# Performance work log

Measured on AMD Instinct MI355X. Metric: run time of the kernel, lower is better.

## Reference

```python
import jax, jax.numpy as jnp
import numpy as np
import math

B, T, D, H = 4, 1024, 1024, 16
DK = D // H
TAU_THRESH = 0.3


def setup_inputs() -> dict:
    key = jax.random.key(0)
    ks = jax.random.split(key, 13)
    s = 1.0 / math.sqrt(D)
    return {
        "x": jax.random.normal(ks[0], (B, T, D), dtype=jnp.float32),
        "Wq": jax.random.normal(ks[1], (D, D), dtype=jnp.float32) * s,
        "bq": jax.random.normal(ks[2], (D,), dtype=jnp.float32) * s,
        "Wk": jax.random.normal(ks[3], (D, D), dtype=jnp.float32) * s,
        "bk": jax.random.normal(ks[4], (D,), dtype=jnp.float32) * s,
        "Wv": jax.random.normal(ks[5], (D, D), dtype=jnp.float32) * s,
        "bv": jax.random.normal(ks[6], (D,), dtype=jnp.float32) * s,
        "Wo": jax.random.normal(ks[7], (D, D), dtype=jnp.float32) * s,
        "bo": jax.random.normal(ks[8], (D,), dtype=jnp.float32) * s,
        "Wg1": jax.random.normal(ks[9], (1, D), dtype=jnp.float32) * s,
        "bg1": jax.random.normal(ks[10], (1,), dtype=jnp.float32) * s,
        "Wg2": jax.random.normal(ks[11], (1, D), dtype=jnp.float32) * s,
        "bg2": jax.random.normal(ks[12], (1,), dtype=jnp.float32) * s,
    }


def reference(x, Wq, bq, Wk, bk, Wv, bv, Wo, bo, Wg1, bg1, Wg2, bg2):
    b, t, d = x.shape
    # projections (torch Linear: y = x @ W.T + b)
    Q = (x @ Wq.T + bq).reshape(b, t, H, DK).transpose(0, 2, 1, 3)  # [B,H,T,dk]
    K = (x @ Wk.T + bk).reshape(b, t, H, DK).transpose(0, 2, 1, 3)
    V = (x @ Wv.T + bv).reshape(b, t, H, DK).transpose(0, 2, 1, 3)
    scores = jnp.einsum("bhqd,bhkd->bhqk", Q, K) / math.sqrt(DK)  # [B,H,T,T]
    # confidence gates from first-token query context [B, H*dk] = [B, D]
    context = Q[:, :, 0, :].reshape(b, d)
    q1 = jax.nn.sigmoid(context @ Wg1.T + bg1)  # [B,1]
    q2 = jax.nn.sigmoid(context @ Wg2.T + bg2)  # [B,1]
    c = jnp.clip(q1 * q2, 1e-8, 1.0)            # [B,1]
    tau = jnp.where(c < TAU_THRESH, 1.0 / c, jnp.ones_like(c)).reshape(b, 1, 1, 1)
    p = jax.nn.softmax(scores / tau, axis=-1)
    cb = c.reshape(b, 1, 1, 1)
    p_gated = cb * p + (1.0 - cb) * (1.0 / t)
    u = jnp.mean(1.0 - c, axis=-1, keepdims=True)  # [B,1]
    attn_out = jnp.einsum("bhqk,bhkd->bhqd", p_gated, V)
    attn_out = attn_out.transpose(0, 2, 1, 3).reshape(b, t, d)
    output = attn_out @ Wo.T + bo
    return output, u
```

## Files before the change

### kernel.cpp

```cpp
#include <hip/hip_runtime.h>
#include <stdint.h>

typedef short bf16x8 __attribute__((ext_vector_type(8)));
typedef float f32x4 __attribute__((ext_vector_type(4)));

#define MFMA_BF16(a, b, c) __builtin_amdgcn_mfma_f32_16x16x32_bf16((a), (b), (c), 0, 0, 0)

__device__ __forceinline__ short f2bf(float x) {
  union { float f; uint32_t u; } v; v.f = x;
  uint32_t r = (v.u + 0x7FFFu + ((v.u >> 16) & 1u)) >> 16;
  return (short)r;
}
__device__ __forceinline__ uint32_t rnd_bf_hi(float x) {
  union { float f; uint32_t u; } v; v.f = x;
  return v.u + 0x7FFFu + ((v.u >> 16) & 1u);
}
__device__ __forceinline__ uint32_t pack2bf(float a, float b) {
  return __builtin_amdgcn_perm(rnd_bf_hi(b), rnd_bf_hi(a), 0x07060302);
}
__device__ __forceinline__ float bfbits2f(uint32_t b16) {
  union { uint32_t u; float f; } v; v.u = b16 << 16; return v.f;
}
__device__ __forceinline__ float fexp2(float x) {
#if __has_builtin(__builtin_amdgcn_exp2f)
  return __builtin_amdgcn_exp2f(x);
#else
  return __expf(x * 0.6931471805599453f);
#endif
}
__device__ __forceinline__ void async16(const void* g, void* l) {
  __builtin_amdgcn_global_load_lds(
      (const __attribute__((address_space(1))) uint32_t*)g,
      (__attribute__((address_space(3))) uint32_t*)l, 16, 0, 0);
}

__global__ __launch_bounds__(256) void prep_k(
    const float* __restrict__ x, const float* __restrict__ Wq,
    const float* __restrict__ Wk, const float* __restrict__ Wv,
    const float* __restrict__ Wo, const float* __restrict__ bq,
    short* __restrict__ xb, short* __restrict__ Wqb, short* __restrict__ Wkb,
    short* __restrict__ Wvb, short* __restrict__ Wob, float* __restrict__ ctx) {
  __shared__ float xs[1024];
  const int bid = blockIdx.x;
  const int tid = threadIdx.x;
  if (bid < 8192) {
    const float* src; short* dst; int idx;
    if (bid < 4096) {
      src = x; dst = xb; idx = (bid << 8) + tid;
    } else {
      const int r = bid - 4096;
      const int z = r >> 10;
      src = (z == 0) ? Wq : (z == 1) ? Wk : (z == 2) ? Wv : Wo;
      dst = (z == 0) ? Wqb : (z == 1) ? Wkb : (z == 2) ? Wvb : Wob;
      idx = ((r & 1023) << 8) + tid;
    }
    float4 v = ((const float4*)src)[idx];
    short4 o;
    o.x = f2bf(v.x); o.y = f2bf(v.y); o.z = f2bf(v.z); o.w = f2bf(v.w);
    ((short4*)dst)[idx] = o;
  } else {
    const int r = bid - 8192;
    const int b = r >> 4;
    const int n0 = (r & 15) << 6;
    for (int i = tid; i < 1024; i += 256) xs[i] = x[b * 1048576 + i];
    __syncthreads();
    const int w = tid >> 6, lane = tid & 63;
    const float4* xv4 = (const float4*)xs;
    for (int rr = 0; rr < 16; ++rr) {
      const int n = n0 + (w << 4) + rr;
      const float4* wrow = (const float4*)(Wq + n * 1024);
      float p = 0.f;
#pragma unroll
      for (int c2 = 0; c2 < 4; ++c2) {
        float4 wv = wrow[lane + (c2 << 6)];
        float4 xv = xv4[lane + (c2 << 6)];
        p += xv.x * wv.x + xv.y * wv.y + xv.z * wv.z + xv.w * wv.w;
      }
#pragma unroll
      for (int off = 32; off; off >>= 1) p += __shfl_xor(p, off);
      if (lane == 0) ctx[b * 1024 + n] = p + bq[n];
    }
  }
}

__global__ __launch_bounds__(256) void gates_fin(const float* __restrict__ ctx,
                                                 const float* __restrict__ Wg1,
                                                 const float* __restrict__ bg1,
                                                 const float* __restrict__ Wg2,
                                                 const float* __restrict__ bg2,
                                                 float* __restrict__ gates,
                                                 float* __restrict__ u_out) {
  __shared__ float red[16];
  const int tid = threadIdx.x, w = tid >> 6, lane = tid & 63;
  for (int b = 0; b < 4; ++b) {
    float4 cv = ((const float4*)(ctx + b * 1024))[tid];
    float4 w1 = ((const float4*)Wg1)[tid];
    float4 w2 = ((const float4*)Wg2)[tid];
    float p1 = cv.x * w1.x + cv.y * w1.y + cv.z * w1.z + cv.w * w1.w;
    float p2 = cv.x * w2.x + cv.y * w2.y + cv.z * w2.z + cv.w * w2.w;
#pragma unroll
    for (int off = 32; off; off >>= 1) { p1 += __shfl_xor(p1, off); p2 += __shfl_xor(p2, off); }
    if (lane == 0) { red[w] = p1; red[8 + w] = p2; }
    __syncthreads();
    if (tid == 0) {
      float g1 = red[0] + red[1] + red[2] + red[3] + bg1[0];
      float g2 = red[8] + red[9] + red[10] + red[11] + bg2[0];
      float q1 = 1.f / (1.f + expf(-g1));
      float q2 = 1.f / (1.f + expf(-g2));
      float c = fminf(fmaxf(q1 * q2, 1e-8f), 1.0f);
      gates[b * 2 + 0] = c;
      gates[b * 2 + 1] = (c < 0.3f ? c : 1.0f) * 0.125f * 1.4426950408889634f;
      u_out[b] = 1.0f - c;
    }
    __syncthreads();
  }
}

template <bool SWP>
__device__ __forceinline__ void qkv_core128(
    const short* __restrict__ A, const short* __restrict__ W,
    const float* __restrict__ bias, short* __restrict__ out,
    short* As, short* Bs, int m0, int n0) {
  const int tid = threadIdx.x;
  const int w = tid >> 6, lane = tid & 63;
  const int m15 = lane & 15, quad = lane >> 4;
  const int wr = w >> 1, wc = w & 1;

  f32x4 acc[4][4];
#pragma unroll
  for (int i = 0; i < 4; ++i)
#pragma unroll
    for (int j = 0; j < 4; ++j) { f32x4 zz = {0.f, 0.f, 0.f, 0.f}; acc[i][j] = zz; }

  const int srow = (w << 5) + (lane >> 2);
  const int sxor = (srow >> 1) & 3;
  const int scol = (((lane & 3) ^ sxor) << 3);
  const short* ga0 = A + (m0 + srow) * 1024 + scol;
  const short* ga1 = ga0 + 16 * 1024;
  const short* gb0 = W + (n0 + srow) * 1024 + scol;
  const short* gb1 = gb0 + 16 * 1024;
  short* la0 = &As[srow * 32 + ((lane & 3) << 3)];
  short* la1 = la0 + 512;
  short* lb0 = &Bs[srow * 32 + ((lane & 3) << 3)];
  short* lb1 = lb0 + 512;

  async16(ga0, la0); async16(ga1, la1);
  async16(gb0, lb0); async16(gb1, lb1);
  __syncthreads();

  for (int kt = 0; kt < 32; ++kt) {
    const int buf = kt & 1;
    if (kt < 31) {
      const int nb = (buf ^ 1) << 12;
      const int off = (kt + 1) << 5;
      async16(ga0 + off, la0 + nb); async16(ga1 + off, la1 + nb);
      async16(gb0 + off, lb0 + nb); async16(gb1 + off, lb1 + nb);
    }
    const short* Ab = As + (buf << 12);
    const short* Bb = Bs + (buf << 12);
    bf16x8 a[4], b[4];
#pragma unroll
    for (int i = 0; i < 4; ++i) {
      const int ra = (wr << 6) + (i << 4) + m15;
      a[i] = *(const bf16x8*)(&Ab[ra * 32 + ((quad ^ ((ra >> 1) & 3)) << 3)]);
    }
#pragma unroll
    for (int j = 0; j < 4; ++j) {
      const int rb = (wc << 6) + (j << 4) + m15;
      b[j] = *(const bf16x8*)(&Bb[rb * 32 + ((quad ^ ((rb >> 1) & 3)) << 3)]);
    }
#pragma unroll
    for (int i = 0; i < 4; ++i)
#pragma unroll
      for (int j = 0; j < 4; ++j) {
        if (SWP) acc[i][j] = MFMA_BF16(b[j], a[i], acc[i][j]);
        else     acc[i][j] = MFMA_BF16(a[i], b[j], acc[i][j]);
      }
    if (kt < 31) __syncthreads();
  }

  if (SWP) {
#pragma unroll
    for (int j = 0; j < 4; ++j) {
      const int n = n0 + (wc << 6) + (j << 4) + (quad << 2);
      const float4 bv = *(const float4*)(bias + n);
      const int hh = n >> 6, dk0 = n & 63;
#pragma unroll
      for (int i = 0; i < 4; ++i) {
        const int m = m0 + (wr << 6) + (i << 4) + m15;
        const int bb = m >> 10, tt = m & 1023;
        uint2 st;
        st.x = pack2bf(acc[i][j][0] + bv.x, acc[i][j][1] + bv.y);
        st.y = pack2bf(acc[i][j][2] + bv.z, acc[i][j][3] + bv.w);
        *(uint2*)(out + (((bb << 4) + hh) << 16) + (tt << 6) + dk0) = st;
      }
    }
  } else {
#pragma unroll
    for (int j = 0; j < 4; ++j) {
      const int n = n0 + (wc << 6) + (j << 4) + m15;
      const float bv = bias[n];
      const int hh = n >> 6, dk = n & 63;
#pragma unroll
      for (int i = 0; i < 4; ++i) {
        const int m = m0 + (wr << 6) + (i << 4) + (quad << 2);
        const int bb = m >> 10, t0 = m & 1023;
        uint2 st;
        st.x = pack2bf(acc[i][j][0] + bv, acc[i][j][1] + bv);
        st.y = pack2bf(acc[i][j][2] + bv, acc[i][j][3] + bv);
        *(uint2*)(out + (((bb << 4) + hh) << 16) + (dk << 10) + t0) = st;
      }
    }
  }
}

__global__ __launch_bounds__(256) void gemm_qkv(
    const short* __restrict__ xb,
    const short* __restrict__ Wqb, const short* __restrict__ Wkb, const short* __restrict__ Wvb,
    const float* __restrict__ bq, const float* __restrict__ bk, const float* __restrict__ bv,
    short* __restrict__ Qh, short* __restrict__ Kh, short* __restrict__ Vt) {
  __shared__ short As[8192];
  __shared__ short Bs[8192];
  const int z = blockIdx.z;
  const int m0 = blockIdx.x << 7, n0 = blockIdx.y << 7;
  if (z == 0)      qkv_core128<true >(xb, Wqb, bq, Qh, As, Bs, m0, n0);
  else if (z == 1) qkv_core128<true >(xb, Wkb, bk, Kh, As, Bs, m0, n0);
  else             qkv_core128<false>(xb, Wvb, bv, Vt, As, Bs, m0, n0);
}

__global__ __launch_bounds__(256) void gemm_out(const short* __restrict__ Ab_,
                                                const short* __restrict__ Wo,
                                                const float* __restrict__ bo,
                                                float* __restrict__ Cout) {
  const int m0 = blockIdx.x << 7;
  const int n0 = blockIdx.y << 7;
  const int tid = threadIdx.x;
  const int w = tid >> 6, lane = tid & 63;
  const int m15 = lane & 15, quad = lane >> 4;
  const int wr = w >> 1, wc = w & 1;

  __shared__ short As[8192];
  __shared__ short Bs[8192];

  f32x4 acc[4][4];
#pragma unroll
  for (int i = 0; i < 4; ++i)
#pragma unroll
    for (int j = 0; j < 4; ++j) { f32x4 zz = {0.f, 0.f, 0.f, 0.f}; acc[i][j] = zz; }

  const int srow = (w << 5) + (lane >> 2);
  const int sxor = (srow >> 1) & 3;
  const int scol = (((lane & 3) ^ sxor) << 3);
  const short* ga0 = Ab_ + (m0 + srow) * 1024 + scol;
  const short* ga1 = ga0 + 16 * 1024;
  const short* gb0 = Wo + (n0 + srow) * 1024 + scol;
  const short* gb1 = gb0 + 16 * 1024;
  short* la0 = &As[srow * 32 + ((lane & 3) << 3)];
  short* la1 = la0 + 512;
  short* lb0 = &Bs[srow * 32 + ((lane & 3) << 3)];
  short* lb1 = lb0 + 512;

  async16(ga0, la0); async16(ga1, la1);
  async16(gb0, lb0); async16(gb1, lb1);
  __syncthreads();

  for (int kt = 0; kt < 32; ++kt) {
    const int buf = kt & 1;
    if (kt < 31) {
      const int nb = (buf ^ 1) << 12;
      const int off = (kt + 1) << 5;
      async16(ga0 + off, la0 + nb); async16(ga1 + off, la1 + nb);
      async16(gb0 + off, lb0 + nb); async16(gb1 + off, lb1 + nb);
    }
    const short* Ab = As + (buf << 12);
    const short* Bb = Bs + (buf << 12);
    bf16x8 a[4], b[4];
#pragma unroll
    for (int i = 0; i < 4; ++i) {
      const int ra = (wr << 6) + (i << 4) + m15;
      a[i] = *(const bf16x8*)(&Ab[ra * 32 + ((quad ^ ((ra >> 1) & 3)) << 3)]);
    }
#pragma unroll
    for (int j = 0; j < 4; ++j) {
      const int rb = (wc << 6) + (j << 4) + m15;
      b[j] = *(const bf16x8*)(&Bb[rb * 32 + ((quad ^ ((rb >> 1) & 3)) << 3)]);
    }
#pragma unroll
    for (int i = 0; i < 4; ++i)
#pragma unroll
      for (int j = 0; j < 4; ++j)
        acc[i][j] = MFMA_BF16(a[i], b[j], acc[i][j]);
    if (kt < 31) __syncthreads();
  }

#pragma unroll
  for (int j = 0; j < 4; ++j) {
    const int n = n0 + (wc << 6) + (j << 4) + m15;
    const float bb_ = bo[n];
#pragma unroll
    for (int i = 0; i < 4; ++i) {
      const int mb = m0 + (wr << 6) + (i << 4) + (quad << 2);
#pragma unroll
      for (int r = 0; r < 4; ++r)
        Cout[(mb + r) * 1024 + n] = acc[i][j][r] + bb_;
    }
  }
}

__global__ __launch_bounds__(256, 2) void attn_k(const short* __restrict__ Qh,
                                                 const short* __restrict__ Kh,
                                                 const short* __restrict__ Vt,
                                                 const float* __restrict__ gates,
                                                 short* __restrict__ attnb) {
  const int bh = blockIdx.x;
  const int b = bh >> 4, h = bh & 15;
  const int q0 = blockIdx.y << 7;
  const int tid = threadIdx.x;
  const int w = tid >> 6, lane = tid & 63;
  const int m15 = lane & 15, quad = lane >> 4;

  __shared__ short Ks[2][4096];
  __shared__ short Vs[3][4096];

  const short* ksrc = Kh + bh * 65536;
  const short* vsrc = Vt + bh * 65536;

  const float sl = gates[b * 2 + 1];

  const short* qsrcA = Qh + ((bh << 10) + q0 + (w << 4) + m15) * 64;
  const short* qsrcB = qsrcA + 64 * 64;
  const bf16x8 qA0 = *(const bf16x8*)(qsrcA + (quad << 3));
  const bf16x8 qA1 = *(const bf16x8*)(qsrcA + 32 + (quad << 3));
  const bf16x8 qB0 = *(const bf16x8*)(qsrcB + (quad << 3));
  const bf16x8 qB1 = *(const bf16x8*)(qsrcB + 32 + (quad << 3));

  const bf16x8 vone = {0x3F80, 0x3F80, 0x3F80, 0x3F80, 0x3F80, 0x3F80, 0x3F80, 0x3F80};

  const int off0 = tid, off1 = tid + 256;
  const int r0 = off0 >> 3, cb0 = (off0 & 7) ^ (r0 & 7);
  const int r1 = off1 >> 3, cb1 = (off1 & 7) ^ (r1 & 7);

#define STAGE(kv, kb, vb)                                                      \
  do {                                                                         \
    async16(ksrc + (((kv) << 6) + r0) * 64 + (cb0 << 3), &Ks[kb][off0 << 3]);  \
    async16(ksrc + (((kv) << 6) + r1) * 64 + (cb1 << 3), &Ks[kb][off1 << 3]);  \
    async16(vsrc + r0 * 1024 + ((kv) << 6) + (cb0 << 3), &Vs[vb][off0 << 3]);  \
    async16(vsrc + r1 * 1024 + ((kv) << 6) + (cb1 << 3), &Vs[vb][off1 << 3]);  \
  } while (0)

  STAGE(0, 0, 0);

  float lsumA = 0.f, lsumB = 0.f;
  f32x4 oA[4], oB[4], o_mv[4];
#pragma unroll
  for (int jd = 0; jd < 4; ++jd) {
    f32x4 zz = {0.f, 0.f, 0.f, 0.f};
    oA[jd] = zz; oB[jd] = zz; o_mv[jd] = zz;
  }

  const int srcA = ((quad & 1) << 5) + m15;
  const int srcB = srcA + 16;
  const bool selhi = (quad & 2) != 0;

#define BUILD_PF(pf, pk)                                                       \
  do {                                                                         \
    _Pragma("unroll")                                                          \
    for (int Hh = 0; Hh < 2; ++Hh) {                                           \
      uint32_t f[4];                                                           \
      _Pragma("unroll")                                                        \
      for (int rp = 0; rp < 2; ++rp) {                                         \
        uint32_t alo = (uint32_t)__shfl((int)pk[2 * Hh][rp], srcA);            \
        uint32_t ahi = (uint32_t)__shfl((int)pk[2 * Hh + 1][rp], srcA);        \
        uint32_t blo = (uint32_t)__shfl((int)pk[2 * Hh][rp], srcB);            \
        uint32_t bhi = (uint32_t)__shfl((int)pk[2 * Hh + 1][rp], srcB);        \
        f[rp]     = selhi ? ahi : alo;                                         \
        f[2 + rp] = selhi ? bhi : blo;                                         \
      }                                                                        \
      pf[Hh] = *(bf16x8*)f;                                                    \
    }                                                                          \
  } while (0)

#define PV_STEP(Vb, pfa, pfb)                                                  \
  do {                                                                         \
    _Pragma("unroll")                                                          \
    for (int jd = 0; jd < 4; ++jd) {                                           \
      const int row = (jd << 4) + m15;                                         \
      const int sw = row & 7;                                                  \
      bf16x8 v0 = *(const bf16x8*)((Vb) + (row << 6) + ((quad ^ sw) << 3));    \
      bf16x8 v1 = *(const bf16x8*)((Vb) + (row << 6) + (((quad + 4) ^ sw) << 3)); \
      oA[jd] = MFMA_BF16(v0, pfa[0], oA[jd]);                                  \
      oA[jd] = MFMA_BF16(v1, pfa[1], oA[jd]);                                  \
      oB[jd] = MFMA_BF16(v0, pfb[0], oB[jd]);                                  \
      oB[jd] = MFMA_BF16(v1, pfb[1], oB[jd]);                                  \
      o_mv[jd] = MFMA_BF16(v0, vone, o_mv[jd]);                                \
      o_mv[jd] = MFMA_BF16(v1, vone, o_mv[jd]);                                \
    }                                                                          \
  } while (0)

  bf16x8 pfpA[2], pfpB[2];
  pfpA[0] = (bf16x8){0,0,0,0,0,0,0,0}; pfpA[1] = pfpA[0];
  pfpB[0] = pfpA[0]; pfpB[1] = pfpA[0];

  for (int kv = 0; kv < 16; ++kv) {
    __syncthreads();
    if (kv < 15) STAGE(kv + 1, (kv + 1) & 1, (kv + 1) % 3);
    const short* Kb = &Ks[kv & 1][0];

    f32x4 sA[4], sB[4];
#pragma unroll
    for (int s = 0; s < 4; ++s) {
      const int row = (s << 4) + m15;
      const int sw = row & 7;
      bf16x8 a0 = *(const bf16x8*)(Kb + (row << 6) + ((quad ^ sw) << 3));
      bf16x8 a1 = *(const bf16x8*)(Kb + (row << 6) + (((quad + 4) ^ sw) << 3));
      f32x4 zA = {0.f, 0.f, 0.f, 0.f};
      zA = MFMA_BF16(a0, qA0, zA);
      zA = MFMA_BF16(a1, qA1, zA);
      sA[s] = zA;
      f32x4 zB = {0.f, 0.f, 0.f, 0.f};
      zB = MFMA_BF16(a0, qB0, zB);
      zB = MFMA_BF16(a1, qB1, zB);
      sB[s] = zB;
    }

    if (kv > 0) {
      const short* Vb = &Vs[(kv - 1) % 3][0];
      PV_STEP(Vb, pfpA, pfpB);
    }

    uint32_t pkA[4][2], pkB[4][2];
#pragma unroll
    for (int s = 0; s < 4; ++s) {
      float a0 = fexp2(sA[s][0] * sl);
      float a1 = fexp2(sA[s][1] * sl);
      float a2 = fexp2(sA[s][2] * sl);
      float a3 = fexp2(sA[s][3] * sl);
      lsumA += (a0 + a1) + (a2 + a3);
      pkA[s][0] = pack2bf(a0, a1);
      pkA[s][1] = pack2bf(a2, a3);
      float b0 = fexp2(sB[s][0] * sl);
      float b1 = fexp2(sB[s][1] * sl);
      float b2 = fexp2(sB[s][2] * sl);
      float b3 = fexp2(sB[s][3] * sl);
      lsumB += (b0 + b1) + (b2 + b3);
      pkB[s][0] = pack2bf(b0, b1);
      pkB[s][1] = pack2bf(b2, b3);
    }

    bf16x8 pfA[2], pfB[2];
    BUILD_PF(pfA, pkA);
    BUILD_PF(pfB, pkB);
    pfpA[0] = pfA[0]; pfpA[1] = pfA[1];
    pfpB[0] = pfB[0]; pfpB[1] = pfB[1];
  }

  {
    const short* Vb = &Vs[15 % 3][0];
    PV_STEP(Vb, pfpA, pfpB);
  }
#undef STAGE
#undef BUILD_PF
#undef PV_STEP

  float lA = lsumA;
  lA += __shfl_xor(lA, 16);
  lA += __shfl_xor(lA, 32);
  float lB = lsumB;
  lB += __shfl_xor(lB, 16);
  lB += __shfl_xor(lB, 32);

  const float cg = gates[b * 2 + 0];
  const float sc0A = cg / lA;
  const float sc0B = cg / lB;
  const float coef = (1.0f - cg) * (1.0f / 1024.0f);
  const int qrowA = q0 + (w << 4) + m15;
  short* orowA = attnb + ((b << 10) + qrowA) * 1024 + (h << 6);
  short* orowB = orowA + 64 * 1024;
#pragma unroll
  for (int jd = 0; jd < 4; ++jd) {
    uint2 stA;
    stA.x = pack2bf(sc0A * oA[jd][0] + coef * o_mv[jd][0],
                    sc0A * oA[jd][1] + coef * o_mv[jd][1]);
    stA.y = pack2bf(sc0A * oA[jd][2] + coef * o_mv[jd][2],
                    sc0A * oA[jd][3] + coef * o_mv[jd][3]);
    *(uint2*)(orowA + (jd << 4) + (quad << 2)) = stA;
    uint2 stB;
    stB.x = pack2bf(sc0B * oB[jd][0] + coef * o_mv[jd][0],
                    sc0B * oB[jd][1] + coef * o_mv[jd][1]);
    stB.y = pack2bf(sc0B * oB[jd][2] + coef * o_mv[jd][2],
                    sc0B * oB[jd][3] + coef * o_mv[jd][3]);
    *(uint2*)(orowB + (jd << 4) + (quad << 2)) = stB;
  }
}

extern "C" void kernel_launch(void* const* d_in, const int* in_sizes, int n_in,
                              void* d_out, int out_size, void* d_ws, size_t ws_size,
                              hipStream_t stream) {
  const float* x   = (const float*)d_in[0];
  const float* Wq  = (const float*)d_in[1];
  const float* bq  = (const float*)d_in[2];
  const float* Wk  = (const float*)d_in[3];
  const float* bk  = (const float*)d_in[4];
  const float* Wv  = (const float*)d_in[5];
  const float* bv  = (const float*)d_in[6];
  const float* Wo  = (const float*)d_in[7];
  const float* bo  = (const float*)d_in[8];
  const float* Wg1 = (const float*)d_in[9];
  const float* bg1 = (const float*)d_in[10];
  const float* Wg2 = (const float*)d_in[11];
  const float* bg2 = (const float*)d_in[12];
  float* out = (float*)d_out;

  char* ws = (char*)d_ws;
  short* xb   = (short*)(ws + 0);
  short* Wqb  = (short*)(ws + 8388608);
  short* Wkb  = (short*)(ws + 10485760);
  short* Wvb  = (short*)(ws + 12582912);
  short* Wob  = (short*)(ws + 14680064);
  short* Qh   = (short*)(ws + 16777216);
  short* Kh   = (short*)(ws + 25165824);
  short* Vt   = (short*)(ws + 33554432);
  short* attb = (short*)(ws + 41943040);
  float* ctx  = (float*)(ws + 50331648);
  float* gat  = (float*)(ws + 50348032);

  prep_k<<<8256, 256, 0, stream>>>(x, Wq, Wk, Wv, Wo, bq,
                                   xb, Wqb, Wkb, Wvb, Wob, ctx);
  gates_fin<<<1, 256, 0, stream>>>(ctx, Wg1, bg1, Wg2, bg2, gat, out + 4194304);

  gemm_qkv<<<dim3(32, 8, 3), 256, 0, stream>>>(xb, Wqb, Wkb, Wvb, bq, bk, bv,
                                               Qh, Kh, Vt);
  attn_k<<<dim3(64, 8), 256, 0, stream>>>(Qh, Kh, Vt, gat, attb);
  gemm_out<<<dim3(32, 8), 256, 0, stream>>>(attb, Wob, bo, out);
}
```

Before: 215.9 us.

## Fuse fp32-to-bf16 conversion into GEMM tile loads and merge gate kernels

Drops the separate conversion pass that wrote bf16 copies of x and all four weight matrices. The QKV and output GEMMs now load fp32 tiles into registers, round them to bf16 and store them into the swizzled LDS double buffer, instead of using async global-to-LDS copies of pre-converted data. The context projection and gate computation are merged into one 4-block kernel that computes all 1024 context rows per batch. This saves a full read/write pass over the converted data and one launch. In exchange, each GEMM tile fetch moves twice the bytes, the loads are staged through registers instead of going async, and the gate kernel runs on only 4 workgroups on the critical path.

```diff
diff --git a/kernel.cpp b/kernel.cpp
--- a/kernel.cpp
+++ b/kernel.cpp
@@ -6,20 +6,12 @@
 
 #define MFMA_BF16(a, b, c) __builtin_amdgcn_mfma_f32_16x16x32_bf16((a), (b), (c), 0, 0, 0)
 
-__device__ __forceinline__ short f2bf(float x) {
-  union { float f; uint32_t u; } v; v.f = x;
-  uint32_t r = (v.u + 0x7FFFu + ((v.u >> 16) & 1u)) >> 16;
-  return (short)r;
-}
 __device__ __forceinline__ uint32_t rnd_bf_hi(float x) {
   union { float f; uint32_t u; } v; v.f = x;
   return v.u + 0x7FFFu + ((v.u >> 16) & 1u);
 }
 __device__ __forceinline__ uint32_t pack2bf(float a, float b) {
   return __builtin_amdgcn_perm(rnd_bf_hi(b), rnd_bf_hi(a), 0x07060302);
-}
-__device__ __forceinline__ float bfbits2f(uint32_t b16) {
-  union { uint32_t u; float f; } v; v.u = b16 << 16; return v.f;
 }
 __device__ __forceinline__ float fexp2(float x) {
 #if __has_builtin(__builtin_amdgcn_exp2f)
@@ -34,91 +26,60 @@
       (__attribute__((address_space(3))) uint32_t*)l, 16, 0, 0);
 }
 
-__global__ __launch_bounds__(256) void prep_k(
+__global__ __launch_bounds__(256) void gates_k(
     const float* __restrict__ x, const float* __restrict__ Wq,
-    const float* __restrict__ Wk, const float* __restrict__ Wv,
-    const float* __restrict__ Wo, const float* __restrict__ bq,
-    short* __restrict__ xb, short* __restrict__ Wqb, short* __restrict__ Wkb,
-    short* __restrict__ Wvb, short* __restrict__ Wob, float* __restrict__ ctx) {
+    const float* __restrict__ bq, const float* __restrict__ Wg1,
+    const float* __restrict__ bg1, const float* __restrict__ Wg2,
+    const float* __restrict__ bg2, float* __restrict__ gates,
+    float* __restrict__ u_out) {
   __shared__ float xs[1024];
-  const int bid = blockIdx.x;
+  __shared__ float ctx[1024];
+  __shared__ float red[16];
+  const int b = blockIdx.x;
   const int tid = threadIdx.x;
-  if (bid < 8192) {
-    const float* src; short* dst; int idx;
-    if (bid < 4096) {
-      src = x; dst = xb; idx = (bid << 8) + tid;
-    } else {
-      const int r = bid - 4096;
-      const int z = r >> 10;
-      src = (z == 0) ? Wq : (z == 1) ? Wk : (z == 2) ? Wv : Wo;
-      dst = (z == 0) ? Wqb : (z == 1) ? Wkb : (z == 2) ? Wvb : Wob;
-      idx = ((r & 1023) << 8) + tid;
-    }
-    float4 v = ((const float4*)src)[idx];
-    short4 o;
-    o.x = f2bf(v.x); o.y = f2bf(v.y); o.z = f2bf(v.z); o.w = f2bf(v.w);
-    ((short4*)dst)[idx] = o;
-  } else {
-    const int r = bid - 8192;
-    const int b = r >> 4;
-    const int n0 = (r & 15) << 6;
-    for (int i = tid; i < 1024; i += 256) xs[i] = x[b * 1048576 + i];
-    __syncthreads();
-    const int w = tid >> 6, lane = tid & 63;
-    const float4* xv4 = (const float4*)xs;
-    for (int rr = 0; rr < 16; ++rr) {
-      const int n = n0 + (w << 4) + rr;
-      const float4* wrow = (const float4*)(Wq + n * 1024);
-      float p = 0.f;
-#pragma unroll
-      for (int c2 = 0; c2 < 4; ++c2) {
-        float4 wv = wrow[lane + (c2 << 6)];
-        float4 xv = xv4[lane + (c2 << 6)];
-        p += xv.x * wv.x + xv.y * wv.y + xv.z * wv.z + xv.w * wv.w;
-      }
-#pragma unroll
-      for (int off = 32; off; off >>= 1) p += __shfl_xor(p, off);
-      if (lane == 0) ctx[b * 1024 + n] = p + bq[n];
-    }
-  }
-}
-
-__global__ __launch_bounds__(256) void gates_fin(const float* __restrict__ ctx,
-                                                 const float* __restrict__ Wg1,
-                                                 const float* __restrict__ bg1,
-                                                 const float* __restrict__ Wg2,
-                                                 const float* __restrict__ bg2,
-                                                 float* __restrict__ gates,
-                                                 float* __restrict__ u_out) {
-  __shared__ float red[16];
-  const int tid = threadIdx.x, w = tid >> 6, lane = tid & 63;
-  for (int b = 0; b < 4; ++b) {
-    float4 cv = ((const float4*)(ctx + b * 1024))[tid];
-    float4 w1 = ((const float4*)Wg1)[tid];
-    float4 w2 = ((const float4*)Wg2)[tid];
-    float p1 = cv.x * w1.x + cv.y * w1.y + cv.z * w1.z + cv.w * w1.w;
-    float p2 = cv.x * w2.x + cv.y * w2.y + cv.z * w2.z + cv.w * w2.w;
-#pragma unroll
-    for (int off = 32; off; off >>= 1) { p1 += __shfl_xor(p1, off); p2 += __shfl_xor(p2, off); }
-    if (lane == 0) { red[w] = p1; red[8 + w] = p2; }
-    __syncthreads();
-    if (tid == 0) {
-      float g1 = red[0] + red[1] + red[2] + red[3] + bg1[0];
-      float g2 = red[8] + red[9] + red[10] + red[11] + bg2[0];
-      float q1 = 1.f / (1.f + expf(-g1));
-      float q2 = 1.f / (1.f + expf(-g2));
-      float c = fminf(fmaxf(q1 * q2, 1e-8f), 1.0f);
-      gates[b * 2 + 0] = c;
-      gates[b * 2 + 1] = (c < 0.3f ? c : 1.0f) * 0.125f * 1.4426950408889634f;
-      u_out[b] = 1.0f - c;
-    }
-    __syncthreads();
+  const int w = tid >> 6, lane = tid & 63;
+  for (int i = tid; i < 1024; i += 256) xs[i] = x[b * 1048576 + i];
+  __syncthreads();
+  const float4* xv4 = (const float4*)xs;
+  for (int rr = 0; rr < 256; ++rr) {
+    const int n = (w << 8) + rr;
+    const float4* wrow = (const float4*)(Wq + n * 1024);
+    float p = 0.f;
+#pragma unroll
+    for (int c2 = 0; c2 < 4; ++c2) {
+      float4 wv = wrow[lane + (c2 << 6)];
+      float4 xv = xv4[lane + (c2 << 6)];
+      p += xv.x * wv.x + xv.y * wv.y + xv.z * wv.z + xv.w * wv.w;
+    }
+#pragma unroll
+    for (int off = 32; off; off >>= 1) p += __shfl_xor(p, off);
+    if (lane == 0) ctx[n] = p + bq[n];
+  }
+  __syncthreads();
+  float4 cv = ((const float4*)ctx)[tid];
+  float4 w1 = ((const float4*)Wg1)[tid];
+  float4 w2 = ((const float4*)Wg2)[tid];
+  float p1 = cv.x * w1.x + cv.y * w1.y + cv.z * w1.z + cv.w * w1.w;
+  float p2 = cv.x * w2.x + cv.y * w2.y + cv.z * w2.z + cv.w * w2.w;
+#pragma unroll
+  for (int off = 32; off; off >>= 1) { p1 += __shfl_xor(p1, off); p2 += __shfl_xor(p2, off); }
+  if (lane == 0) { red[w] = p1; red[8 + w] = p2; }
+  __syncthreads();
+  if (tid == 0) {
+    float g1 = red[0] + red[1] + red[2] + red[3] + bg1[0];
+    float g2 = red[8] + red[9] + red[10] + red[11] + bg2[0];
+    float q1 = 1.f / (1.f + expf(-g1));
+    float q2 = 1.f / (1.f + expf(-g2));
+    float c = fminf(fmaxf(q1 * q2, 1e-8f), 1.0f);
+    gates[b * 2 + 0] = c;
+    gates[b * 2 + 1] = (c < 0.3f ? c : 1.0f) * 0.125f * 1.4426950408889634f;
+    u_out[b] = 1.0f - c;
   }
 }
 
 template <bool SWP>
 __device__ __forceinline__ void qkv_core128(
-    const short* __restrict__ A, const short* __restrict__ W,
+    const float* __restrict__ A, const float* __restrict__ W,
     const float* __restrict__ bias, short* __restrict__ out,
     short* As, short* Bs, int m0, int n0) {
   const int tid = threadIdx.x;
@@ -133,29 +94,52 @@
     for (int j = 0; j < 4; ++j) { f32x4 zz = {0.f, 0.f, 0.f, 0.f}; acc[i][j] = zz; }
 
   const int srow = (w << 5) + (lane >> 2);
-  const int sxor = (srow >> 1) & 3;
-  const int scol = (((lane & 3) ^ sxor) << 3);
-  const short* ga0 = A + (m0 + srow) * 1024 + scol;
-  const short* ga1 = ga0 + 16 * 1024;
-  const short* gb0 = W + (n0 + srow) * 1024 + scol;
-  const short* gb1 = gb0 + 16 * 1024;
-  short* la0 = &As[srow * 32 + ((lane & 3) << 3)];
-  short* la1 = la0 + 512;
-  short* lb0 = &Bs[srow * 32 + ((lane & 3) << 3)];
-  short* lb1 = lb0 + 512;
-
-  async16(ga0, la0); async16(ga1, la1);
-  async16(gb0, lb0); async16(gb1, lb1);
+  const int chk = lane & 3;
+  const int pchk = chk ^ ((srow >> 1) & 3);
+  const float* gA0 = A + (m0 + srow) * 1024 + (chk << 3);
+  const float* gA1 = gA0 + 16384;
+  const float* gB0 = W + (n0 + srow) * 1024 + (chk << 3);
+  const float* gB1 = gB0 + 16384;
+  short* lA0 = &As[srow * 32 + (pchk << 3)];
+  short* lA1 = lA0 + 512;
+  short* lB0 = &Bs[srow * 32 + (pchk << 3)];
+  short* lB1 = lB0 + 512;
+
+  float4 ra0, ra1, ra2, ra3, rb0, rb1, rb2, rb3;
+
+#define LOADT(t)                                                 \
+  do {                                                           \
+    const float4* pa0 = (const float4*)(gA0 + ((t) << 5));       \
+    const float4* pa1 = (const float4*)(gA1 + ((t) << 5));       \
+    const float4* pb0 = (const float4*)(gB0 + ((t) << 5));       \
+    const float4* pb1 = (const float4*)(gB1 + ((t) << 5));       \
+    ra0 = pa0[0]; ra1 = pa0[1]; ra2 = pa1[0]; ra3 = pa1[1];      \
+    rb0 = pb0[0]; rb1 = pb0[1]; rb2 = pb1[0]; rb3 = pb1[1];      \
+  } while (0)
+
+#define WRITET(bi)                                                            \
+  do {                                                                        \
+    *(uint4*)(lA0 + ((bi) << 12)) =                                           \
+        make_uint4(pack2bf(ra0.x, ra0.y), pack2bf(ra0.z, ra0.w),              \
+                   pack2bf(ra1.x, ra1.y), pack2bf(ra1.z, ra1.w));             \
+    *(uint4*)(lA1 + ((bi) << 12)) =                                           \
+        make_uint4(pack2bf(ra2.x, ra2.y), pack2bf(ra2.z, ra2.w),              \
+                   pack2bf(ra3.x, ra3.y), pack2bf(ra3.z, ra3.w));             \
+    *(uint4*)(lB0 + ((bi) << 12)) =                                           \
+        make_uint4(pack2bf(rb0.x, rb0.y), pack2bf(rb0.z, rb0.w),              \
+                   pack2bf(rb1.x, rb1.y), pack2bf(rb1.z, rb1.w));             \
+    *(uint4*)(lB1 + ((bi) << 12)) =                                           \
+        make_uint4(pack2bf(rb2.x, rb2.y), pack2bf(rb2.z, rb2.w),              \
+                   pack2bf(rb3.x, rb3.y), pack2bf(rb3.z, rb3.w));             \
+  } while (0)
+
+  LOADT(0);
+  WRITET(0);
   __syncthreads();
 
   for (int kt = 0; kt < 32; ++kt) {
     const int buf = kt & 1;
-    if (kt < 31) {
-      const int nb = (buf ^ 1) << 12;
-      const int off = (kt + 1) << 5;
-      async16(ga0 + off, la0 + nb); async16(ga1 + off, la1 + nb);
-      async16(gb0 + off, lb0 + nb); async16(gb1 + off, lb1 + nb);
-    }
+    if (kt < 31) LOADT(kt + 1);
     const short* Ab = As + (buf << 12);
     const short* Bb = Bs + (buf << 12);
     bf16x8 a[4], b[4];
@@ -176,8 +160,13 @@
         if (SWP) acc[i][j] = MFMA_BF16(b[j], a[i], acc[i][j]);
         else     acc[i][j] = MFMA_BF16(a[i], b[j], acc[i][j]);
       }
-    if (kt < 31) __syncthreads();
-  }
+    if (kt < 31) {
+      WRITET(buf ^ 1);
+      __syncthreads();
+    }
+  }
+#undef LOADT
+#undef WRITET
 
   if (SWP) {
 #pragma unroll
@@ -215,21 +204,21 @@
 }
 
 __global__ __launch_bounds__(256) void gemm_qkv(
-    const short* __restrict__ xb,
-    const short* __restrict__ Wqb, const short* __restrict__ Wkb, const short* __restrict__ Wvb,
+    const float* __restrict__ x,
+    const float* __restrict__ Wq, const float* __restrict__ Wk, const float* __restrict__ Wv,
     const float* __restrict__ bq, const float* __restrict__ bk, const float* __restrict__ bv,
     short* __restrict__ Qh, short* __restrict__ Kh, short* __restrict__ Vt) {
   __shared__ short As[8192];
   __shared__ short Bs[8192];
   const int z = blockIdx.z;
   const int m0 = blockIdx.x << 7, n0 = blockIdx.y << 7;
-  if (z == 0)      qkv_core128<true >(xb, Wqb, bq, Qh, As, Bs, m0, n0);
-  else if (z == 1) qkv_core128<true >(xb, Wkb, bk, Kh, As, Bs, m0, n0);
-  else             qkv_core128<false>(xb, Wvb, bv, Vt, As, Bs, m0, n0);
+  if (z == 0)      qkv_core128<true >(x, Wq, bq, Qh, As, Bs, m0, n0);
+  else if (z == 1) qkv_core128<true >(x, Wk, bk, Kh, As, Bs, m0, n0);
+  else             qkv_core128<false>(x, Wv, bv, Vt, As, Bs, m0, n0);
 }
 
 __global__ __launch_bounds__(256) void gemm_out(const short* __restrict__ Ab_,
-                                                const short* __restrict__ Wo,
+                                                const float* __restrict__ Wo,
                                                 const float* __restrict__ bo,
                                                 float* __restrict__ Cout) {
   const int m0 = blockIdx.x << 7;
@@ -250,18 +239,39 @@
 
   const int srow = (w << 5) + (lane >> 2);
   const int sxor = (srow >> 1) & 3;
-  const int scol = (((lane & 3) ^ sxor) << 3);
-  const short* ga0 = Ab_ + (m0 + srow) * 1024 + scol;
+  const int chk = lane & 3;
+  const int pchk = chk ^ sxor;
+  const short* ga0 = Ab_ + (m0 + srow) * 1024 + (pchk << 3);
   const short* ga1 = ga0 + 16 * 1024;
-  const short* gb0 = Wo + (n0 + srow) * 1024 + scol;
-  const short* gb1 = gb0 + 16 * 1024;
-  short* la0 = &As[srow * 32 + ((lane & 3) << 3)];
+  short* la0 = &As[srow * 32 + (chk << 3)];
   short* la1 = la0 + 512;
-  short* lb0 = &Bs[srow * 32 + ((lane & 3) << 3)];
-  short* lb1 = lb0 + 512;
+  const float* gB0 = Wo + (n0 + srow) * 1024 + (chk << 3);
+  const float* gB1 = gB0 + 16384;
+  short* lB0 = &Bs[srow * 32 + (pchk << 3)];
+  short* lB1 = lB0 + 512;
+
+  float4 rb0, rb1, rb2, rb3;
+
+#define LOADB(t)                                                 \
+  do {                                                           \
+    const float4* pb0 = (const float4*)(gB0 + ((t) << 5));       \
+    const float4* pb1 = (const float4*)(gB1 + ((t) << 5));       \
+    rb0 = pb0[0]; rb1 = pb0[1]; rb2 = pb1[0]; rb3 = pb1[1];      \
+  } while (0)
+
+#define WRITEB(bi)                                                            \
+  do {                                                                        \
+    *(uint4*)(lB0 + ((bi) << 12)) =                                           \
+        make_uint4(pack2bf(rb0.x, rb0.y), pack2bf(rb0.z, rb0.w),              \
+                   pack2bf(rb1.x, rb1.y), pack2bf(rb1.z, rb1.w));             \
+    *(uint4*)(lB1 + ((bi) << 12)) =                                           \
+        make_uint4(pack2bf(rb2.x, rb2.y), pack2bf(rb2.z, rb2.w),              \
+                   pack2bf(rb3.x, rb3.y), pack2bf(rb3.z, rb3.w));             \
+  } while (0)
 
   async16(ga0, la0); async16(ga1, la1);
-  async16(gb0, lb0); async16(gb1, lb1);
+  LOADB(0);
+  WRITEB(0);
   __syncthreads();
 
   for (int kt = 0; kt < 32; ++kt) {
@@ -270,7 +280,7 @@
       const int nb = (buf ^ 1) << 12;
       const int off = (kt + 1) << 5;
       async16(ga0 + off, la0 + nb); async16(ga1 + off, la1 + nb);
-      async16(gb0 + off, lb0 + nb); async16(gb1 + off, lb1 + nb);
+      LOADB(kt + 1);
     }
     const short* Ab = As + (buf << 12);
     const short* Bb = Bs + (buf << 12);
@@ -290,8 +300,13 @@
 #pragma unroll
       for (int j = 0; j < 4; ++j)
         acc[i][j] = MFMA_BF16(a[i], b[j], acc[i][j]);
-    if (kt < 31) __syncthreads();
-  }
+    if (kt < 31) {
+      WRITEB(buf ^ 1);
+      __syncthreads();
+    }
+  }
+#undef LOADB
+#undef WRITEB
 
 #pragma unroll
   for (int j = 0; j < 4; ++j) {
@@ -512,24 +527,16 @@
   float* out = (float*)d_out;
 
   char* ws = (char*)d_ws;
-  short* xb   = (short*)(ws + 0);
-  short* Wqb  = (short*)(ws + 8388608);
-  short* Wkb  = (short*)(ws + 10485760);
-  short* Wvb  = (short*)(ws + 12582912);
-  short* Wob  = (short*)(ws + 14680064);
-  short* Qh   = (short*)(ws + 16777216);
-  short* Kh   = (short*)(ws + 25165824);
-  short* Vt   = (short*)(ws + 33554432);
-  short* attb = (short*)(ws + 41943040);
-  float* ctx  = (float*)(ws + 50331648);
-  float* gat  = (float*)(ws + 50348032);
-
-  prep_k<<<8256, 256, 0, stream>>>(x, Wq, Wk, Wv, Wo, bq,
-                                   xb, Wqb, Wkb, Wvb, Wob, ctx);
-  gates_fin<<<1, 256, 0, stream>>>(ctx, Wg1, bg1, Wg2, bg2, gat, out + 4194304);
-
-  gemm_qkv<<<dim3(32, 8, 3), 256, 0, stream>>>(xb, Wqb, Wkb, Wvb, bq, bk, bv,
+  short* Qh   = (short*)(ws + 0);
+  short* Kh   = (short*)(ws + 8388608);
+  short* Vt   = (short*)(ws + 16777216);
+  short* attb = (short*)(ws + 25165824);
+  float* gat  = (float*)(ws + 33554432);
+
+  gates_k<<<4, 256, 0, stream>>>(x, Wq, bq, Wg1, bg1, Wg2, bg2, gat,
+                                 out + 4194304);
+  gemm_qkv<<<dim3(32, 8, 3), 256, 0, stream>>>(x, Wq, Wk, Wv, bq, bk, bv,
                                                Qh, Kh, Vt);
   attn_k<<<dim3(64, 8), 256, 0, stream>>>(Qh, Kh, Vt, gat, attb);
-  gemm_out<<<dim3(32, 8), 256, 0, stream>>>(attb, Wob, bo, out);
-}
+  gemm_out<<<dim3(32, 8), 256, 0, stream>>>(attb, Wo, bo, out);
+}
```

Measured after the change: 398.5 us. +84.6%, slower.
